# Optimization experiments

Hardware: AMD Instinct MI355X
Metric: run time of the kernel (lower is better)

## Reference

```python
import jax, jax.numpy as jnp
import numpy as np

N = 100000
E = 1600000
NFEAT = 256
NHID = 128
LATENT = 64


def setup_inputs() -> dict:
    key = jax.random.key(0)
    ks = jax.random.split(key, 12)
    x = jax.random.normal(ks[0], (N, NFEAT), dtype=jnp.float32)
    edge_index = jax.random.randint(ks[1], (2, E), 0, N, dtype=jnp.int32)
    edge_weight = jax.random.uniform(ks[2], (E,), dtype=jnp.float32)
    # GraphConvolution params: uniform(-stdv, stdv), stdv = 1/sqrt(out_features)
    s1 = 1.0 / np.sqrt(NHID)
    gc1_w = jax.random.uniform(ks[3], (NFEAT, NHID), minval=-s1, maxval=s1, dtype=jnp.float32)
    gc1_b = jax.random.uniform(ks[4], (NHID,), minval=-s1, maxval=s1, dtype=jnp.float32)
    gc2_w = jax.random.uniform(ks[5], (NHID, NHID), minval=-s1, maxval=s1, dtype=jnp.float32)
    gc2_b = jax.random.uniform(ks[6], (NHID,), minval=-s1, maxval=s1, dtype=jnp.float32)
    # nn.Linear default init: uniform(-1/sqrt(fan_in), 1/sqrt(fan_in))
    s2 = 1.0 / np.sqrt(NHID)
    mu_w = jax.random.uniform(ks[7], (NHID, LATENT), minval=-s2, maxval=s2, dtype=jnp.float32)
    mu_b = jax.random.uniform(ks[8], (LATENT,), minval=-s2, maxval=s2, dtype=jnp.float32)
    lv_w = jax.random.uniform(ks[9], (NHID, LATENT), minval=-s2, maxval=s2, dtype=jnp.float32)
    lv_b = jax.random.uniform(ks[10], (LATENT,), minval=-s2, maxval=s2, dtype=jnp.float32)
    return {"x": x, "edge_index": edge_index, "edge_weight": edge_weight,
            "gc1_w": gc1_w, "gc1_b": gc1_b, "gc2_w": gc2_w, "gc2_b": gc2_b,
            "mu_w": mu_w, "mu_b": mu_b, "lv_w": lv_w, "lv_b": lv_b}


def _spmm(edge_index, edge_weight, support):
    # out[row] += w * support[col]  (sparse adj @ dense support)
    row, col = edge_index[0], edge_index[1]
    msgs = support[col] * edge_weight[:, None]          # [E, F]
    return jax.ops.segment_sum(msgs, row, num_segments=N)


def reference(x, edge_index, edge_weight, gc1_w, gc1_b, gc2_w, gc2_b,
              mu_w, mu_b, lv_w, lv_b):
    # gc1: mm -> spmm -> bias -> relu (dropout is identity in eval mode)
    h = jax.nn.relu(_spmm(edge_index, edge_weight, x @ gc1_w) + gc1_b)
    h = jax.nn.relu(_spmm(edge_index, edge_weight, h @ gc2_w) + gc2_b)
    mu = h @ mu_w + mu_b
    log_var = h @ lv_w + lv_b
    return mu, log_var
```

## Files before the change

kernel.cpp:

```cpp
#include <hip/hip_runtime.h>
#include <hip/hip_fp16.h>

#define N_NODES 100000
#define N_EDGES 1600000
#define NFEAT   256
#define NHID    128
#define LATENT  64

#define NBUCKET 782
#define NBLKH   196
#define CHUNK   8192
#define NHIST   (NBUCKET * NBLKH)
#define NHISTT  300

typedef __attribute__((ext_vector_type(8))) short s16x8;
typedef __attribute__((ext_vector_type(4))) float f32x4;

__device__ __forceinline__ unsigned short f2bf(float f) {
    union { float f; unsigned u; } v; v.f = f;
    unsigned r = v.u + 0x7fffu + ((v.u >> 16) & 1u);
    return (unsigned short)(r >> 16);
}
__device__ __forceinline__ float bflo(unsigned u) {
    union { unsigned x; float f; } v; v.x = u << 16; return v.f;
}
__device__ __forceinline__ float bfhi(unsigned u) {
    union { unsigned x; float f; } v; v.x = u & 0xffff0000u; return v.f;
}
__device__ __forceinline__ float w15_decode(unsigned pv) {
    return __half2float(__ushort_as_half((unsigned short)(pv & 0x7fffu)));
}

__device__ __forceinline__ int incl_scan512(int v, int t, int (&s)[2][512]) {
    s[0][t] = v;
    __syncthreads();
    int p = 0;
    for (int off = 1; off < 512; off <<= 1) {
        int x = s[p][t];
        if (t >= off) x += s[p][t - off];
        s[p ^ 1][t] = x;
        p ^= 1;
        __syncthreads();
    }
    return s[p][t];
}


__device__ __forceinline__ void prep_body(
    int c, int K, int Ntot, int ncol0, int ldb0, int ldb1,
    const float* __restrict__ B0, const float* __restrict__ B1,
    unsigned short* __restrict__ out)
{
    int K8 = K >> 3;
    int total = (Ntot >> 4) * K8 * 16;
    if (c >= total) return;
    int m  = c & 15;
    int kc = (c >> 4) % K8;
    int nt = (c >> 4) / K8;
    int col = nt * 16 + m;
    const float* src; int ld, cc;
    if (col < ncol0) { src = B0; ld = ldb0; cc = col; }
    else             { src = B1; ld = ldb1; cc = col - ncol0; }
    s16x8 v;
    #pragma unroll
    for (int j = 0; j < 8; ++j)
        v[j] = (short)f2bf(src[(size_t)(kc * 8 + j) * ld + cc]);
    *(s16x8*)&out[(size_t)c * 8] = v;
}


__global__ __launch_bounds__(256) void k_pre(
    const int* __restrict__ rows, int* __restrict__ histG,
    const float* __restrict__ gc1_w, unsigned short* __restrict__ w1p,
    const float* __restrict__ gc2_w, unsigned short* __restrict__ w2p,
    const float* __restrict__ mu_w, const float* __restrict__ lv_w,
    unsigned short* __restrict__ w3p)
{
    int b = blockIdx.x;
    int t = threadIdx.x;
    if (b < NBLKH) {
        __shared__ int hist[NBUCKET];
        for (int i = t; i < NBUCKET; i += 256) hist[i] = 0;
        __syncthreads();
        int base = b * CHUNK;
        #pragma unroll 4
        for (int i = 0; i < CHUNK / 256; ++i) {
            int e = base + i * 256 + t;
            if (e < N_EDGES) {
                int r = rows[e];
                atomicAdd(&hist[r >> 7], 1);
            }
        }
        __syncthreads();
        for (int i = t; i < NBUCKET; i += 256)
            histG[(size_t)i * NBLKH + b] = hist[i];
    } else if (b < NBLKH + 16) {
        prep_body((b - NBLKH) * 256 + t, NFEAT, NHID, NHID, NHID, NHID, gc1_w, gc1_w, w1p);
    } else if (b < NBLKH + 24) {
        prep_body((b - NBLKH - 16) * 256 + t, NHID, NHID, NHID, NHID, NHID, gc2_w, gc2_w, w2p);
    } else {
        prep_body((b - NBLKH - 24) * 256 + t, NHID, NHID, LATENT, LATENT, LATENT, mu_w, lv_w, w3p);
    }
}


__global__ __launch_bounds__(512) void k_scanA(
    const int* __restrict__ histG, int* __restrict__ hist_excl,
    int* __restrict__ hbsum)
{
    __shared__ int s[2][512];
    int b = blockIdx.x, t = threadIdx.x;
    int i = b * 512 + t;
    int v = (i < NHIST) ? histG[i] : 0;
    int incl = incl_scan512(v, t, s);
    if (i < NHIST) hist_excl[i] = incl - v;
    if (t == 511) hbsum[b] = incl;
}

__global__ __launch_bounds__(512) void k_scanC(
    const int* __restrict__ hist_excl, const int* __restrict__ hbsum,
    int* __restrict__ scanned)
{
    __shared__ int s[2][512];
    __shared__ int sbase;
    int b = blockIdx.x, t = threadIdx.x;
    int v = (t < NHISTT) ? hbsum[t] : 0;
    int incl = incl_scan512(v, t, s);
    if (t == b) sbase = incl - v;
    __syncthreads();
    int base = sbase;
    int i = b * 512 + t;
    if (i < NHIST) scanned[i] = hist_excl[i] + base;
}


__global__ __launch_bounds__(256) void k_scatterA(
    const int* __restrict__ rows, const int* __restrict__ cols,
    const float* __restrict__ ew, const int* __restrict__ scanned,
    uint2* __restrict__ tmp)
{
    __shared__ int cur[NBUCKET];
    int b = blockIdx.x, t = threadIdx.x;
    for (int i = t; i < NBUCKET; i += 256)
        cur[i] = scanned[(size_t)i * NBLKH + b];
    __syncthreads();
    int base = b * CHUNK;
    #pragma unroll 4
    for (int i = 0; i < CHUNK / 256; ++i) {
        int e = base + i * 256 + t;
        if (e < N_EDGES) {
            int r = rows[e];
            unsigned hv = (unsigned)__half_as_ushort(__float2half(ew[e]));
            unsigned pv = ((unsigned)cols[e] << 15) | (hv & 0x7fffu);
            int p = atomicAdd(&cur[r >> 7], 1);
            tmp[p] = make_uint2(pv, (unsigned)r);
        }
    }
}


__global__ __launch_bounds__(256) void k_passB(
    const int* __restrict__ scanned, const uint2* __restrict__ tmp,
    unsigned* __restrict__ ecw, int* __restrict__ row_ptr)
{
    __shared__ int cnt[128];
    __shared__ int sc[2][128];
    __shared__ int cur[128];
    int b  = blockIdx.x;
    int t  = threadIdx.x;
    int r0 = b * 128;
    int beg = scanned[(size_t)b * NBLKH];
    int end = (b + 1 < NBUCKET) ? scanned[(size_t)(b + 1) * NBLKH] : N_EDGES;
    if (t < 128) cnt[t] = 0;
    __syncthreads();
    for (int e = beg + t; e < end; e += 256)
        atomicAdd(&cnt[tmp[e].y & 127], 1);
    __syncthreads();
    int p = 0;
    if (t < 128) sc[0][t] = cnt[t];
    __syncthreads();
    for (int off = 1; off < 128; off <<= 1) {
        if (t < 128) {
            int x = sc[p][t];
            if (t >= off) x += sc[p][t - off];
            sc[p ^ 1][t] = x;
        }
        p ^= 1;
        __syncthreads();
    }
    if (t < 128) {
        int excl = sc[p][t] - cnt[t];
        int rr = r0 + t;
        if (rr < N_NODES) row_ptr[rr] = beg + excl;
        cur[t] = beg + excl;
    }
    if (b == NBUCKET - 1 && t == 0) row_ptr[N_NODES] = N_EDGES;
    __syncthreads();
    for (int e = beg + t; e < end; e += 256) {
        uint2 v = tmp[e];
        int pos = atomicAdd(&cur[v.y & 127], 1);
        ecw[pos] = v.x;
    }
}


template<int AMODE, int OMODE>
__global__ __launch_bounds__(256) void k_gemm(
    int K, const float* __restrict__ A32, const unsigned short* __restrict__ A16,
    const unsigned short* __restrict__ Bpre,
    unsigned short* __restrict__ C16,
    float* __restrict__ C0, float* __restrict__ C1,
    const float* __restrict__ bias0, const float* __restrict__ bias1)
{
    __shared__ unsigned short As[2048];
    __shared__ unsigned short Bs[8192];

    const int t    = threadIdx.x;
    const int m0   = blockIdx.x * 32;
    const int lane = t & 63;
    const int w    = t >> 6;
    const int rt   = w & 1;
    const int ntb  = (w >> 1) * 4;
    const int fm   = lane & 15;
    const int q    = lane >> 4;
    const int K8   = K >> 3;

    f32x4 acc[4] = {};

    for (int kt = 0; kt < K; kt += 64) {
        {
            int r = t >> 3, kc = t & 7;
            int lo = ((r >> 4) * 8 + kc) * 128 + (r & 15) * 8;
            if (AMODE == 0) {
                const float* g = A32 + (size_t)(m0 + r) * K + kt + kc * 8;
                float4 a = *(const float4*)g;
                float4 b = *(const float4*)(g + 4);
                s16x8 v;
                v[0] = (short)f2bf(a.x); v[1] = (short)f2bf(a.y);
                v[2] = (short)f2bf(a.z); v[3] = (short)f2bf(a.w);
                v[4] = (short)f2bf(b.x); v[5] = (short)f2bf(b.y);
                v[6] = (short)f2bf(b.z); v[7] = (short)f2bf(b.w);
                *(s16x8*)&As[lo] = v;
            } else {
                const unsigned short* g = A16 + (size_t)(m0 + r) * 128 + kt + kc * 8;
                *(s16x8*)&As[lo] = *(const s16x8*)g;
            }
        }
        {
            int ktc = kt >> 3;
            #pragma unroll
            for (int i = 0; i < 4; ++i) {
                int c  = t + i * 256;
                int nt = c >> 7, kc = (c >> 4) & 7, m = c & 15;
                const unsigned short* g =
                    Bpre + ((size_t)(nt * K8 + ktc + kc) * 16 + m) * 8;
                *(s16x8*)&Bs[c * 8] = *(const s16x8*)g;
            }
        }
        __syncthreads();
        #pragma unroll
        for (int kk = 0; kk < 2; ++kk) {
            int kcq = kk * 4 + q;
            s16x8 a = *(const s16x8*)&As[(rt * 8 + kcq) * 128 + fm * 8];
            #pragma unroll
            for (int i = 0; i < 4; ++i) {
                s16x8 b = *(const s16x8*)&Bs[((ntb + i) * 8 + kcq) * 128 + fm * 8];
                acc[i] = __builtin_amdgcn_mfma_f32_16x16x32_bf16(a, b, acc[i], 0, 0, 0);
            }
        }
        __syncthreads();
    }

    #pragma unroll
    for (int i = 0; i < 4; ++i) {
        int col = (ntb + i) * 16 + fm;
        #pragma unroll
        for (int j = 0; j < 4; ++j) {
            int r = m0 + rt * 16 + q * 4 + j;
            float v = acc[i][j];
            if (OMODE == 0) {
                C16[(size_t)r * 128 + col] = f2bf(v);
            } else {
                if (col < 64) C0[(size_t)r * 64 + col]      = v + bias0[col];
                else          C1[(size_t)r * 64 + col - 64] = v + bias1[col - 64];
            }
        }
    }
}


#define EDGE8(qq, vv, A)                                  \
    {                                                     \
        float ww = w15_decode(qq);                        \
        A[0] += ww * bflo(vv.x); A[1] += ww * bfhi(vv.x); \
        A[2] += ww * bflo(vv.y); A[3] += ww * bfhi(vv.y); \
        A[4] += ww * bflo(vv.z); A[5] += ww * bfhi(vv.z); \
        A[6] += ww * bflo(vv.w); A[7] += ww * bfhi(vv.w); \
    }

__global__ __launch_bounds__(256) void k_spmm(const int* __restrict__ row_ptr,
                                              const unsigned* __restrict__ ecw,
                                              const unsigned short* __restrict__ sup,
                                              const float* __restrict__ bias,
                                              unsigned short* __restrict__ out) {
    int wave = threadIdx.x >> 6;
    int lane = threadIdx.x & 63;
    int row  = blockIdx.x * 4 + wave;
    if (row >= N_NODES) return;
    int g  = lane >> 4;
    int fl = lane & 15;

    int beg = row_ptr[row];
    int end = row_ptr[row + 1];
    float a[8] = {}, b[8] = {};

    int e = beg;
    for (; e + 16 <= end; e += 16) {
        unsigned q0 = ecw[e + g];
        unsigned q1 = ecw[e + 4 + g];
        unsigned q2 = ecw[e + 8 + g];
        unsigned q3 = ecw[e + 12 + g];
        uint4 v0 = *(const uint4*)(sup + (size_t)(q0 >> 15) * NHID + fl * 8);
        uint4 v1 = *(const uint4*)(sup + (size_t)(q1 >> 15) * NHID + fl * 8);
        uint4 v2 = *(const uint4*)(sup + (size_t)(q2 >> 15) * NHID + fl * 8);
        uint4 v3 = *(const uint4*)(sup + (size_t)(q3 >> 15) * NHID + fl * 8);
        EDGE8(q0, v0, a)
        EDGE8(q1, v1, b)
        EDGE8(q2, v2, a)
        EDGE8(q3, v3, b)
    }
    for (; e + 8 <= end; e += 8) {
        unsigned q0 = ecw[e + g];
        unsigned q1 = ecw[e + 4 + g];
        uint4 v0 = *(const uint4*)(sup + (size_t)(q0 >> 15) * NHID + fl * 8);
        uint4 v1 = *(const uint4*)(sup + (size_t)(q1 >> 15) * NHID + fl * 8);
        EDGE8(q0, v0, a)
        EDGE8(q1, v1, b)
    }
    if (e < end) {
        int last = end - 1;
        int e0 = e + g, e1 = e + 4 + g;
        unsigned q0 = ecw[e0 <= last ? e0 : last];
        unsigned q1 = ecw[e1 <= last ? e1 : last];
        uint4 v0 = *(const uint4*)(sup + (size_t)(q0 >> 15) * NHID + fl * 8);
        uint4 v1 = *(const uint4*)(sup + (size_t)(q1 >> 15) * NHID + fl * 8);
        float w0 = (e0 <= last) ? w15_decode(q0) : 0.f;
        float w1 = (e1 <= last) ? w15_decode(q1) : 0.f;
        a[0] += w0 * bflo(v0.x); a[1] += w0 * bfhi(v0.x);
        a[2] += w0 * bflo(v0.y); a[3] += w0 * bfhi(v0.y);
        a[4] += w0 * bflo(v0.z); a[5] += w0 * bfhi(v0.z);
        a[6] += w0 * bflo(v0.w); a[7] += w0 * bfhi(v0.w);
        b[0] += w1 * bflo(v1.x); b[1] += w1 * bfhi(v1.x);
        b[2] += w1 * bflo(v1.y); b[3] += w1 * bfhi(v1.y);
        b[4] += w1 * bflo(v1.z); b[5] += w1 * bfhi(v1.z);
        b[6] += w1 * bflo(v1.w); b[7] += w1 * bfhi(v1.w);
    }

    #pragma unroll
    for (int k = 0; k < 8; ++k) {
        float v = a[k] + b[k];
        v += __shfl_xor(v, 16, 64);
        v += __shfl_xor(v, 32, 64);
        a[k] = v;
    }

    if (lane < 16) {
        uint4 pv;
        unsigned o[8];
        #pragma unroll
        for (int k = 0; k < 8; ++k) {
            float v = a[k] + bias[fl * 8 + k];
            v = v > 0.f ? v : 0.f;
            o[k] = (unsigned)f2bf(v);
        }
        pv.x = o[0] | (o[1] << 16);
        pv.y = o[2] | (o[3] << 16);
        pv.z = o[4] | (o[5] << 16);
        pv.w = o[6] | (o[7] << 16);
        *(uint4*)(out + (size_t)row * NHID + fl * 8) = pv;
    }
}


extern "C" void kernel_launch(void* const* d_in, const int* in_sizes, int n_in,
                              void* d_out, int out_size, void* d_ws, size_t ws_size,
                              hipStream_t stream) {
    const float* x     = (const float*)d_in[0];
    const int*   ei    = (const int*)  d_in[1];
    const float* ew    = (const float*)d_in[2];
    const float* gc1_w = (const float*)d_in[3];
    const float* gc1_b = (const float*)d_in[4];
    const float* gc2_w = (const float*)d_in[5];
    const float* gc2_b = (const float*)d_in[6];
    const float* mu_w  = (const float*)d_in[7];
    const float* mu_b  = (const float*)d_in[8];
    const float* lv_w  = (const float*)d_in[9];
    const float* lv_b  = (const float*)d_in[10];
    float* out = (float*)d_out;

    const int* rows = ei;
    const int* cols = ei + N_EDGES;

    char* p = (char*)d_ws;
    auto alloc = [&](size_t bytes) {
        char* r = p;
        p += (bytes + 255) & ~(size_t)255;
        return r;
    };
    int*      row_ptr   = (int*)     alloc((size_t)(N_NODES + 1) * 4);
    int*      histG     = (int*)     alloc((size_t)NHIST * 4);
    int*      hist_excl = (int*)     alloc((size_t)NHIST * 4);
    int*      hbsum     = (int*)     alloc((size_t)NHISTT * 4);
    int*      scanned   = (int*)     alloc((size_t)NHIST * 4);
    unsigned* ecw       = (unsigned*)alloc((size_t)N_EDGES * 4);
    uint2*    tmp       = (uint2*)   alloc((size_t)N_EDGES * 8);
    unsigned short* w1p    = (unsigned short*)alloc((size_t)NFEAT * NHID * 2);
    unsigned short* w2p    = (unsigned short*)alloc((size_t)NHID * NHID * 2);
    unsigned short* w3p    = (unsigned short*)alloc((size_t)NHID * NHID * 2);
    unsigned short* bufSup = (unsigned short*)alloc((size_t)N_NODES * NHID * 2);
    unsigned short* bufH   = (unsigned short*)alloc((size_t)N_NODES * NHID * 2);
    (void)ws_size; (void)n_in; (void)in_sizes; (void)out_size;

    k_pre<<<NBLKH + 32, 256, 0, stream>>>(rows, histG,
                                          gc1_w, w1p, gc2_w, w2p, mu_w, lv_w, w3p);
    k_scanA<<<NHISTT, 512, 0, stream>>>(histG, hist_excl, hbsum);
    k_scanC<<<NHISTT, 512, 0, stream>>>(hist_excl, hbsum, scanned);
    k_scatterA<<<NBLKH, 256, 0, stream>>>(rows, cols, ew, scanned, tmp);
    k_passB<<<NBUCKET, 256, 0, stream>>>(scanned, tmp, ecw, row_ptr);

    k_gemm<0, 0><<<N_NODES / 32, 256, 0, stream>>>(NFEAT, x, nullptr, w1p,
                                                   bufSup, nullptr, nullptr, nullptr, nullptr);
    k_spmm<<<N_NODES / 4, 256, 0, stream>>>(row_ptr, ecw, bufSup, gc1_b, bufH);
    k_gemm<1, 0><<<N_NODES / 32, 256, 0, stream>>>(NHID, nullptr, bufH, w2p,
                                                   bufSup, nullptr, nullptr, nullptr, nullptr);
    k_spmm<<<N_NODES / 4, 256, 0, stream>>>(row_ptr, ecw, bufSup, gc2_b, bufH);
    k_gemm<1, 1><<<N_NODES / 32, 256, 0, stream>>>(NHID, nullptr, bufH, w3p,
                                                   nullptr, out, out + (size_t)N_NODES * LATENT,
                                                   mu_b, lv_b);
}
```

Measured before the change: 419.4 us.

## Fuse CSR build into one cooperative kernel with grid syncs

Replaces the five preprocessing kernels (histogram, two scan passes, bucket scatter, per-row pass) with a single cooperative kernel that uses grid-wide syncs between phases. The edge chunk shrinks so there are as many histogram blocks as buckets, which lets the two-level scan become a 782x782 matrix scan done per block. The aim is to remove kernel launch gaps and the tail idle time between small kernels. The cost is grid sync overhead and more, smaller blocks. The cooperative launch also needs all 814 blocks to be resident at once, and its return value is not checked.

After: 747.4 us. 78.2% more time.

```diff
diff --git a/kernel.cpp b/kernel.cpp
--- a/kernel.cpp
+++ b/kernel.cpp
@@ -1,5 +1,8 @@
 #include <hip/hip_runtime.h>
 #include <hip/hip_fp16.h>
+#include <hip/hip_cooperative_groups.h>
+
+namespace cg = cooperative_groups;
 
 #define N_NODES 100000
 #define N_EDGES 1600000
@@ -8,10 +11,8 @@
 #define LATENT  64
 
 #define NBUCKET 782
-#define NBLKH   196
-#define CHUNK   8192
-#define NHIST   (NBUCKET * NBLKH)
-#define NHISTT  300
+#define CH2     2048
+#define NPREP   32
 
 typedef __attribute__((ext_vector_type(8))) short s16x8;
 typedef __attribute__((ext_vector_type(4))) float f32x4;
@@ -29,20 +30,6 @@
 }
 __device__ __forceinline__ float w15_decode(unsigned pv) {
     return __half2float(__ushort_as_half((unsigned short)(pv & 0x7fffu)));
-}
-
-__device__ __forceinline__ int incl_scan512(int v, int t, int (&s)[2][512]) {
-    s[0][t] = v;
-    __syncthreads();
-    int p = 0;
-    for (int off = 1; off < 512; off <<= 1) {
-        int x = s[p][t];
-        if (t >= off) x += s[p][t - off];
-        s[p ^ 1][t] = x;
-        p ^= 1;
-        __syncthreads();
-    }
-    return s[p][t];
 }
 
 
@@ -68,138 +55,141 @@
     *(s16x8*)&out[(size_t)c * 8] = v;
 }
 
-
-__global__ __launch_bounds__(256) void k_pre(
-    const int* __restrict__ rows, int* __restrict__ histG,
+__device__ __forceinline__ int scan782(int (&sB)[2][NBUCKET], int t) {
+    int p = 0;
+    for (int off = 1; off < NBUCKET; off <<= 1) {
+        for (int i = t; i < NBUCKET; i += 256) {
+            int x = sB[p][i];
+            if (i >= off) x += sB[p][i - off];
+            sB[p ^ 1][i] = x;
+        }
+        p ^= 1;
+        __syncthreads();
+    }
+    return p;
+}
+
+
+__global__ __launch_bounds__(256) void k_reorder(
+    const int* __restrict__ rows, const int* __restrict__ cols,
+    const float* __restrict__ ew,
+    int* __restrict__ histG, int* __restrict__ bsum,
+    int* __restrict__ bucket_start,
+    uint2* __restrict__ tmp, unsigned* __restrict__ ecw,
+    int* __restrict__ row_ptr,
     const float* __restrict__ gc1_w, unsigned short* __restrict__ w1p,
     const float* __restrict__ gc2_w, unsigned short* __restrict__ w2p,
     const float* __restrict__ mu_w, const float* __restrict__ lv_w,
     unsigned short* __restrict__ w3p)
 {
+    cg::grid_group gg = cg::this_grid();
+    __shared__ int sA[NBUCKET];
+    __shared__ int sB[2][NBUCKET];
+    __shared__ int sCurB[NBUCKET];
+    __shared__ int sCnt[128], sS[2][128], sCur[128];
+
     int b = blockIdx.x;
     int t = threadIdx.x;
-    if (b < NBLKH) {
-        __shared__ int hist[NBUCKET];
-        for (int i = t; i < NBUCKET; i += 256) hist[i] = 0;
-        __syncthreads();
-        int base = b * CHUNK;
-        #pragma unroll 4
-        for (int i = 0; i < CHUNK / 256; ++i) {
+
+    if (b < NBUCKET) {
+        for (int i = t; i < NBUCKET; i += 256) sA[i] = 0;
+        __syncthreads();
+        int base = b * CH2;
+        #pragma unroll
+        for (int i = 0; i < CH2 / 256; ++i) {
+            int e = base + i * 256 + t;
+            if (e < N_EDGES) atomicAdd(&sA[rows[e] >> 7], 1);
+        }
+        __syncthreads();
+        for (int i = t; i < NBUCKET; i += 256)
+            histG[(size_t)i * NBUCKET + b] = sA[i];
+    } else if (b < NBUCKET + 16) {
+        prep_body((b - NBUCKET) * 256 + t, NFEAT, NHID, NHID, NHID, NHID,
+                  gc1_w, gc1_w, w1p);
+    } else if (b < NBUCKET + 24) {
+        prep_body((b - NBUCKET - 16) * 256 + t, NHID, NHID, NHID, NHID, NHID,
+                  gc2_w, gc2_w, w2p);
+    } else {
+        prep_body((b - NBUCKET - 24) * 256 + t, NHID, NHID, LATENT, LATENT,
+                  LATENT, mu_w, lv_w, w3p);
+    }
+    gg.sync();
+
+    if (b < NBUCKET) {
+        for (int i = t; i < NBUCKET; i += 256)
+            sB[0][i] = histG[(size_t)b * NBUCKET + i];
+        __syncthreads();
+        int p = scan782(sB, t);
+        for (int i = t; i < NBUCKET; i += 256) {
+            int v = histG[(size_t)b * NBUCKET + i];
+            histG[(size_t)b * NBUCKET + i] = sB[p][i] - v;
+        }
+        if (t == 0) bsum[b] = sB[p][NBUCKET - 1];
+    }
+    gg.sync();
+
+    if (b < NBUCKET) {
+        for (int i = t; i < NBUCKET; i += 256) sB[0][i] = bsum[i];
+        __syncthreads();
+        int p = scan782(sB, t);
+        for (int i = t; i < NBUCKET; i += 256) {
+            int excl = sB[p][i] - bsum[i];
+            sA[i] = excl;
+            if (b == 0) bucket_start[i] = excl;
+        }
+        __syncthreads();
+        for (int i = t; i < NBUCKET; i += 256)
+            sCurB[i] = sA[i] + histG[(size_t)i * NBUCKET + b];
+        __syncthreads();
+        int base = b * CH2;
+        #pragma unroll
+        for (int i = 0; i < CH2 / 256; ++i) {
             int e = base + i * 256 + t;
             if (e < N_EDGES) {
                 int r = rows[e];
-                atomicAdd(&hist[r >> 7], 1);
-            }
-        }
-        __syncthreads();
-        for (int i = t; i < NBUCKET; i += 256)
-            histG[(size_t)i * NBLKH + b] = hist[i];
-    } else if (b < NBLKH + 16) {
-        prep_body((b - NBLKH) * 256 + t, NFEAT, NHID, NHID, NHID, NHID, gc1_w, gc1_w, w1p);
-    } else if (b < NBLKH + 24) {
-        prep_body((b - NBLKH - 16) * 256 + t, NHID, NHID, NHID, NHID, NHID, gc2_w, gc2_w, w2p);
-    } else {
-        prep_body((b - NBLKH - 24) * 256 + t, NHID, NHID, LATENT, LATENT, LATENT, mu_w, lv_w, w3p);
-    }
-}
-
-
-__global__ __launch_bounds__(512) void k_scanA(
-    const int* __restrict__ histG, int* __restrict__ hist_excl,
-    int* __restrict__ hbsum)
-{
-    __shared__ int s[2][512];
-    int b = blockIdx.x, t = threadIdx.x;
-    int i = b * 512 + t;
-    int v = (i < NHIST) ? histG[i] : 0;
-    int incl = incl_scan512(v, t, s);
-    if (i < NHIST) hist_excl[i] = incl - v;
-    if (t == 511) hbsum[b] = incl;
-}
-
-__global__ __launch_bounds__(512) void k_scanC(
-    const int* __restrict__ hist_excl, const int* __restrict__ hbsum,
-    int* __restrict__ scanned)
-{
-    __shared__ int s[2][512];
-    __shared__ int sbase;
-    int b = blockIdx.x, t = threadIdx.x;
-    int v = (t < NHISTT) ? hbsum[t] : 0;
-    int incl = incl_scan512(v, t, s);
-    if (t == b) sbase = incl - v;
-    __syncthreads();
-    int base = sbase;
-    int i = b * 512 + t;
-    if (i < NHIST) scanned[i] = hist_excl[i] + base;
-}
-
-
-__global__ __launch_bounds__(256) void k_scatterA(
-    const int* __restrict__ rows, const int* __restrict__ cols,
-    const float* __restrict__ ew, const int* __restrict__ scanned,
-    uint2* __restrict__ tmp)
-{
-    __shared__ int cur[NBUCKET];
-    int b = blockIdx.x, t = threadIdx.x;
-    for (int i = t; i < NBUCKET; i += 256)
-        cur[i] = scanned[(size_t)i * NBLKH + b];
-    __syncthreads();
-    int base = b * CHUNK;
-    #pragma unroll 4
-    for (int i = 0; i < CHUNK / 256; ++i) {
-        int e = base + i * 256 + t;
-        if (e < N_EDGES) {
-            int r = rows[e];
-            unsigned hv = (unsigned)__half_as_ushort(__float2half(ew[e]));
-            unsigned pv = ((unsigned)cols[e] << 15) | (hv & 0x7fffu);
-            int p = atomicAdd(&cur[r >> 7], 1);
-            tmp[p] = make_uint2(pv, (unsigned)r);
-        }
-    }
-}
-
-
-__global__ __launch_bounds__(256) void k_passB(
-    const int* __restrict__ scanned, const uint2* __restrict__ tmp,
-    unsigned* __restrict__ ecw, int* __restrict__ row_ptr)
-{
-    __shared__ int cnt[128];
-    __shared__ int sc[2][128];
-    __shared__ int cur[128];
-    int b  = blockIdx.x;
-    int t  = threadIdx.x;
-    int r0 = b * 128;
-    int beg = scanned[(size_t)b * NBLKH];
-    int end = (b + 1 < NBUCKET) ? scanned[(size_t)(b + 1) * NBLKH] : N_EDGES;
-    if (t < 128) cnt[t] = 0;
-    __syncthreads();
-    for (int e = beg + t; e < end; e += 256)
-        atomicAdd(&cnt[tmp[e].y & 127], 1);
-    __syncthreads();
-    int p = 0;
-    if (t < 128) sc[0][t] = cnt[t];
-    __syncthreads();
-    for (int off = 1; off < 128; off <<= 1) {
+                unsigned hv = (unsigned)__half_as_ushort(__float2half(ew[e]));
+                unsigned pv = ((unsigned)cols[e] << 15) | (hv & 0x7fffu);
+                int pos = atomicAdd(&sCurB[r >> 7], 1);
+                tmp[pos] = make_uint2(pv, (unsigned)r);
+            }
+        }
+    }
+    gg.sync();
+
+    if (b < NBUCKET) {
+        int r0 = b * 128;
+        int beg = bucket_start[b];
+        int end = (b + 1 < NBUCKET) ? bucket_start[b + 1] : N_EDGES;
+        if (t < 128) sCnt[t] = 0;
+        __syncthreads();
+        for (int e = beg + t; e < end; e += 256)
+            atomicAdd(&sCnt[tmp[e].y & 127], 1);
+        __syncthreads();
+        int p = 0;
+        if (t < 128) sS[0][t] = sCnt[t];
+        __syncthreads();
+        for (int off = 1; off < 128; off <<= 1) {
+            if (t < 128) {
+                int x = sS[p][t];
+                if (t >= off) x += sS[p][t - off];
+                sS[p ^ 1][t] = x;
+            }
+            p ^= 1;
+            __syncthreads();
+        }
         if (t < 128) {
-            int x = sc[p][t];
-            if (t >= off) x += sc[p][t - off];
-            sc[p ^ 1][t] = x;
-        }
-        p ^= 1;
-        __syncthreads();
-    }
-    if (t < 128) {
-        int excl = sc[p][t] - cnt[t];
-        int rr = r0 + t;
-        if (rr < N_NODES) row_ptr[rr] = beg + excl;
-        cur[t] = beg + excl;
-    }
-    if (b == NBUCKET - 1 && t == 0) row_ptr[N_NODES] = N_EDGES;
-    __syncthreads();
-    for (int e = beg + t; e < end; e += 256) {
-        uint2 v = tmp[e];
-        int pos = atomicAdd(&cur[v.y & 127], 1);
-        ecw[pos] = v.x;
+            int excl = sS[p][t] - sCnt[t];
+            int rr = r0 + t;
+            if (rr < N_NODES) row_ptr[rr] = beg + excl;
+            sCur[t] = beg + excl;
+        }
+        if (b == 0 && t == 0) row_ptr[N_NODES] = N_EDGES;
+        __syncthreads();
+        for (int e = beg + t; e < end; e += 256) {
+            uint2 v = tmp[e];
+            int pos = atomicAdd(&sCur[v.y & 127], 1);
+            ecw[pos] = v.x;
+        }
     }
 }
 
@@ -407,13 +397,12 @@
         p += (bytes + 255) & ~(size_t)255;
         return r;
     };
-    int*      row_ptr   = (int*)     alloc((size_t)(N_NODES + 1) * 4);
-    int*      histG     = (int*)     alloc((size_t)NHIST * 4);
-    int*      hist_excl = (int*)     alloc((size_t)NHIST * 4);
-    int*      hbsum     = (int*)     alloc((size_t)NHISTT * 4);
-    int*      scanned   = (int*)     alloc((size_t)NHIST * 4);
-    unsigned* ecw       = (unsigned*)alloc((size_t)N_EDGES * 4);
-    uint2*    tmp       = (uint2*)   alloc((size_t)N_EDGES * 8);
+    int*      row_ptr      = (int*)     alloc((size_t)(N_NODES + 1) * 4);
+    int*      histG        = (int*)     alloc((size_t)NBUCKET * NBUCKET * 4);
+    int*      bsum         = (int*)     alloc((size_t)NBUCKET * 4);
+    int*      bucket_start = (int*)     alloc((size_t)NBUCKET * 4);
+    unsigned* ecw          = (unsigned*)alloc((size_t)N_EDGES * 4);
+    uint2*    tmp          = (uint2*)   alloc((size_t)N_EDGES * 8);
     unsigned short* w1p    = (unsigned short*)alloc((size_t)NFEAT * NHID * 2);
     unsigned short* w2p    = (unsigned short*)alloc((size_t)NHID * NHID * 2);
     unsigned short* w3p    = (unsigned short*)alloc((size_t)NHID * NHID * 2);
@@ -421,12 +410,15 @@
     unsigned short* bufH   = (unsigned short*)alloc((size_t)N_NODES * NHID * 2);
     (void)ws_size; (void)n_in; (void)in_sizes; (void)out_size;
 
-    k_pre<<<NBLKH + 32, 256, 0, stream>>>(rows, histG,
-                                          gc1_w, w1p, gc2_w, w2p, mu_w, lv_w, w3p);
-    k_scanA<<<NHISTT, 512, 0, stream>>>(histG, hist_excl, hbsum);
-    k_scanC<<<NHISTT, 512, 0, stream>>>(hist_excl, hbsum, scanned);
-    k_scatterA<<<NBLKH, 256, 0, stream>>>(rows, cols, ew, scanned, tmp);
-    k_passB<<<NBUCKET, 256, 0, stream>>>(scanned, tmp, ecw, row_ptr);
+    void* kargs[] = {
+        (void*)&rows, (void*)&cols, (void*)&ew,
+        (void*)&histG, (void*)&bsum, (void*)&bucket_start,
+        (void*)&tmp, (void*)&ecw, (void*)&row_ptr,
+        (void*)&gc1_w, (void*)&w1p, (void*)&gc2_w, (void*)&w2p,
+        (void*)&mu_w, (void*)&lv_w, (void*)&w3p
+    };
+    hipLaunchCooperativeKernel((void*)k_reorder, dim3(NBUCKET + NPREP),
+                               dim3(256), kargs, 0, stream);
 
     k_gemm<0, 0><<<N_NODES / 32, 256, 0, stream>>>(NFEAT, x, nullptr, w1p,
                                                    bufSup, nullptr, nullptr, nullptr, nullptr);
```
